# Kernel optimization log

Hardware: AMD Instinct MI355X
Metric: run time of the kernel (lower is better)

## Reference

```python
import jax, jax.numpy as jnp
import numpy as np

# tree structure: B trees, layer sizes per tree 2048 -> 256 -> 32 -> 1 (arities 8, 8, 32)
B = 256
N0, N1, N2, N3 = B * 2048, B * 256, B * 32, B * 1
D_IN, HID, OUT = 128, 256, 10
EPS = 1e-5


def _bn(x, g, b):
    # BatchNorm1d, training-mode batch stats (biased variance), as in torch
    mu = jnp.mean(x, axis=0)
    var = jnp.var(x, axis=0)
    return (x - mu) * jax.lax.rsqrt(var + EPS) * g + b


def _tree_layer(pooled, w1, b1, bn1g, bn1b, w2, b2, bng, bnb):
    # MLP(2 layers): Linear -> BN -> ReLU -> Linear, then outer BN -> ReLU (next_layer)
    z = jax.nn.relu(_bn(pooled @ w1 + b1, bn1g, bn1b))
    z = z @ w2 + b2
    return jax.nn.relu(_bn(z, bng, bnb))


def setup_inputs() -> dict:
    key = jax.random.key(0)
    ks = jax.random.split(key, 12)
    s = 0.05
    ar = lambda n: jnp.arange(n, dtype=jnp.int32)
    inp = {
        'x': jax.random.normal(ks[0], (N0, D_IN), jnp.float32),
        # child -> parent index (global, trees are contiguous blocks)
        'parent1': ar(N0) // 8,
        'parent2': ar(N1) // 8,
        'parent3': ar(N2) // 32,
        # node -> tree id per layer (for sum tree-pooling readout)
        'tree0': ar(N0) // 2048,
        'tree1': ar(N1) // 256,
        'tree2': ar(N2) // 32,
        # layer 1 MLP (input_dim -> hidden)
        'l1_w1': jax.random.normal(ks[1], (D_IN, HID), jnp.float32) * s,
        'l1_b1': jnp.zeros((HID,), jnp.float32),
        'l1_bn1g': jnp.ones((HID,), jnp.float32),
        'l1_bn1b': jnp.zeros((HID,), jnp.float32),
        'l1_w2': jax.random.normal(ks[2], (HID, HID), jnp.float32) * s,
        'l1_b2': jnp.zeros((HID,), jnp.float32),
        'l1_bng': jnp.ones((HID,), jnp.float32),
        'l1_bnb': jnp.zeros((HID,), jnp.float32),
        # layers 2 and 3 MLPs (hidden -> hidden), stacked on axis 0
        'lw1': jax.random.normal(ks[3], (2, HID, HID), jnp.float32) * s,
        'lb1': jnp.zeros((2, HID), jnp.float32),
        'lbn1g': jnp.ones((2, HID), jnp.float32),
        'lbn1b': jnp.zeros((2, HID), jnp.float32),
        'lw2': jax.random.normal(ks[4], (2, HID, HID), jnp.float32) * s,
        'lb2': jnp.zeros((2, HID), jnp.float32),
        'lbng': jnp.ones((2, HID), jnp.float32),
        'lbnb': jnp.zeros((2, HID), jnp.float32),
        # prediction heads
        'pred0_w': jax.random.normal(ks[5], (D_IN, OUT), jnp.float32) * s,
        'pred0_b': jnp.zeros((OUT,), jnp.float32),
        'predh_w': jax.random.normal(ks[6], (3, HID, OUT), jnp.float32) * s,
        'predh_b': jnp.zeros((3, OUT), jnp.float32),
    }
    return inp


def reference(x, parent1, parent2, parent3, tree0, tree1, tree2,
              l1_w1, l1_b1, l1_bn1g, l1_bn1b, l1_w2, l1_b2, l1_bng, l1_bnb,
              lw1, lb1, lbn1g, lbn1b, lw2, lb2, lbng, lbnb,
              pred0_w, pred0_b, predh_w, predh_b):
    seg = jax.ops.segment_sum
    h0 = x
    # layer 1: sparse child pooling (spmm == segment_sum) + MLP + BN + ReLU
    h1 = _tree_layer(seg(h0, parent1, num_segments=N1),
                     l1_w1, l1_b1, l1_bn1g, l1_bn1b, l1_w2, l1_b2, l1_bng, l1_bnb)
    h2 = _tree_layer(seg(h1, parent2, num_segments=N2),
                     lw1[0], lb1[0], lbn1g[0], lbn1b[0], lw2[0], lb2[0], lbng[0], lbnb[0])
    h3 = _tree_layer(seg(h2, parent3, num_segments=N3),
                     lw1[1], lb1[1], lbn1g[1], lbn1b[1], lw2[1], lb2[1], lbng[1], lbnb[1])
    # sum tree-pooling readout over layers 0..depth-1, plus root-layer linear
    score = seg(h0, tree0, num_segments=B) @ pred0_w + pred0_b
    score = score + seg(h1, tree1, num_segments=B) @ predh_w[0] + predh_b[0]
    score = score + seg(h2, tree2, num_segments=B) @ predh_w[1] + predh_b[1]
    score = score + h3 @ predh_w[2] + predh_b[2]  # h3 has 1 root per tree -> [B, OUT]
    return score
```

## Files before the change

### kernel.cpp

```cpp
#include <hip/hip_runtime.h>
#include <hip/hip_bf16.h>


#define N0 (256*2048)
#define N1 (256*256)
#define N2 (256*32)
#define NB 256
#define BN_EPS 1e-5f
#define NSLOT 8

typedef __attribute__((ext_vector_type(8))) __bf16 bf16x8;
typedef __attribute__((ext_vector_type(8))) unsigned short u16x8;
typedef __attribute__((ext_vector_type(4))) unsigned short u16x4;
typedef __attribute__((ext_vector_type(4))) float f32x4;

__device__ inline float bf2f(unsigned short b) {
    unsigned u = ((unsigned)b) << 16;
    float f; __builtin_memcpy(&f, &u, 4); return f;
}
__device__ inline unsigned short f2bf(float f) {
    unsigned u; __builtin_memcpy(&u, &f, 4);
    u += 0x7fff + ((u >> 16) & 1);
    return (unsigned short)(u >> 16);
}

__global__ __launch_bounds__(256) void prep_weights(const float* __restrict__ l1_w1,
                                                    const float* __restrict__ l1_w2,
                                                    const float* __restrict__ lw1,
                                                    const float* __restrict__ lw2,
                                                    unsigned short* __restrict__ Wt) {
    int idx = blockIdx.x * 256 + threadIdx.x;
    if (idx >= 360448) return;
    float v;
    if (idx < 32768) {
        int n = idx >> 7, k = idx & 127;
        v = l1_w1[k * 256 + n];
    } else if (idx < 98304) {
        int j = idx - 32768, n = j >> 8, k = j & 255;
        v = l1_w2[k * 256 + n];
    } else if (idx < 163840) {
        int j = idx - 98304, n = j >> 8, k = j & 255;
        v = lw1[k * 256 + n];
    } else if (idx < 229376) {
        int j = idx - 163840, n = j >> 8, k = j & 255;
        v = lw2[k * 256 + n];
    } else if (idx < 294912) {
        int j = idx - 229376, n = j >> 8, k = j & 255;
        v = lw1[65536 + k * 256 + n];
    } else {
        int j = idx - 294912, n = j >> 8, k = j & 255;
        v = lw2[65536 + k * 256 + n];
    }
    Wt[idx] = f2bf(v);
}

__device__ inline void bn_prologue(int tid, const float* __restrict__ partials,
                                   const float* __restrict__ g, const float* __restrict__ b,
                                   float invM, float* sc_lds, float* sh_lds) {
    if (tid < 256) {
        float s = 0.f, s2 = 0.f;
#pragma unroll
        for (int k = 0; k < NSLOT; ++k) {
            s  += partials[k * 512 + tid];
            s2 += partials[k * 512 + 256 + tid];
        }
        float mean = s * invM;
        float var = s2 * invM - mean * mean;
        float sc = g[tid] * rsqrtf(var + BN_EPS);
        sc_lds[tid] = sc;
        sh_lds[tid] = b[tid] - mean * sc;
    }
}

__global__ __launch_bounds__(512) void gemm1_fused(const float* __restrict__ x,
                                                   const unsigned short* __restrict__ Wt,
                                                   const float* __restrict__ bias,
                                                   unsigned short* __restrict__ Z1,
                                                   float* __restrict__ stat_partials,
                                                   float* __restrict__ ts0) {
    constexpr int LDA = 136, LDB = 72;
    __shared__ unsigned short Asb[128 * LDA];
    __shared__ unsigned short Bsb[256 * LDB];
    const int tid = threadIdx.x;
    const int c4 = tid & 31, rg = tid >> 5;
    const int m0 = blockIdx.x * 128;
    const int tree = blockIdx.x >> 1;
    f32x4 colp = {0.f, 0.f, 0.f, 0.f};
#pragma unroll
    for (int i = 0; i < 8; ++i) {
        int row = rg * 8 + i;
        const f32x4* xp = reinterpret_cast<const f32x4*>(x + (size_t)(m0 + row) * 1024 + c4 * 4);
        f32x4 s = {0.f, 0.f, 0.f, 0.f};
#pragma unroll
        for (int c = 0; c < 8; ++c) s += xp[c * 32];
        u16x4 o;
#pragma unroll
        for (int e = 0; e < 4; ++e) o[e] = f2bf(s[e]);
        *reinterpret_cast<u16x4*>(&Asb[row * LDA + c4 * 4]) = o;
        colp += s;
    }
#pragma unroll
    for (int e = 0; e < 4; ++e) atomicAdd(&ts0[tree * 128 + c4 * 4 + e], colp[e]);

    const int wave = tid >> 6, lane = tid & 63;
    const int q = lane >> 4, r = lane & 15;
    const int wc = wave & 3, wr = wave >> 2;
    f32x4 acc[4][4];
#pragma unroll
    for (int i = 0; i < 4; ++i)
#pragma unroll
        for (int j = 0; j < 4; ++j) acc[i][j] = (f32x4){0.f, 0.f, 0.f, 0.f};

#pragma unroll
    for (int s2 = 0; s2 < 2; ++s2) {
#pragma unroll
        for (int i = 0; i < 4; ++i) {
            int v = tid + i * 512;
            int n = v >> 3, kc = v & 7;
            u16x8 d = *reinterpret_cast<const u16x8*>(Wt + (size_t)n * 128 + s2 * 64 + kc * 8);
            *reinterpret_cast<u16x8*>(&Bsb[n * LDB + kc * 8]) = d;
        }
        __syncthreads();
#pragma unroll
        for (int s = 0; s < 2; ++s) {
            bf16x8 a[4], b[4];
#pragma unroll
            for (int i = 0; i < 4; ++i)
                a[i] = *reinterpret_cast<const bf16x8*>(&Asb[(wr * 64 + i * 16 + r) * LDA + s2 * 64 + s * 32 + q * 8]);
#pragma unroll
            for (int j = 0; j < 4; ++j)
                b[j] = *reinterpret_cast<const bf16x8*>(&Bsb[(wc * 64 + j * 16 + r) * LDB + s * 32 + q * 8]);
#pragma unroll
            for (int i = 0; i < 4; ++i)
#pragma unroll
                for (int j = 0; j < 4; ++j)
                    acc[i][j] = __builtin_amdgcn_mfma_f32_16x16x32_bf16(a[i], b[j], acc[i][j], 0, 0, 0);
        }
        __syncthreads();
    }
    float sj[4], s2j[4];
#pragma unroll
    for (int j = 0; j < 4; ++j) {
        float bj = bias[wc * 64 + j * 16 + r];
        float s = 0.f, s2 = 0.f;
#pragma unroll
        for (int i = 0; i < 4; ++i)
#pragma unroll
            for (int e = 0; e < 4; ++e) {
                acc[i][j][e] += bj;
                float v = acc[i][j][e];
                s += v; s2 += v * v;
            }
        s  += __shfl_xor(s, 16);  s  += __shfl_xor(s, 32);
        s2 += __shfl_xor(s2, 16); s2 += __shfl_xor(s2, 32);
        sj[j] = s; s2j[j] = s2;
    }
#pragma unroll
    for (int i = 0; i < 4; ++i)
#pragma unroll
        for (int e = 0; e < 4; ++e) {
            size_t row = m0 + wr * 64 + i * 16 + q * 4 + e;
#pragma unroll
            for (int j = 0; j < 4; ++j)
                Z1[row * 256 + wc * 64 + j * 16 + r] = f2bf(acc[i][j][e]);
        }
    if (q == 0) {
        int slot = blockIdx.x & (NSLOT - 1);
#pragma unroll
        for (int j = 0; j < 4; ++j) {
            int col = wc * 64 + j * 16 + r;
            atomicAdd(&stat_partials[slot * 512 + col], sj[j]);
            atomicAdd(&stat_partials[slot * 512 + 256 + col], s2j[j]);
        }
    }
}

__global__ __launch_bounds__(256) void gemm2_fused(const unsigned short* __restrict__ Z2,
                                                   const float* __restrict__ partials_in,
                                                   const float* __restrict__ bn_g,
                                                   const float* __restrict__ bn_b,
                                                   float invM,
                                                   const unsigned short* __restrict__ Wt2,
                                                   const float* __restrict__ bias,
                                                   unsigned short* __restrict__ Z2a,
                                                   float* __restrict__ stat_partials,
                                                   float* __restrict__ ts1) {
    constexpr int LDA = 264, LDB = 72;
    __shared__ unsigned short Asb[64 * LDA];
    __shared__ unsigned short Bsb[256 * LDB];
    __shared__ float sc_lds[256], sh_lds[256];
    const int tid = threadIdx.x;
    bn_prologue(tid, partials_in, bn_g, bn_b, invM, sc_lds, sh_lds);
    __syncthreads();
    const int c8 = tid & 31, rg = tid >> 5;
    const int m0 = blockIdx.x * 64;
    const int d0 = c8 * 8;
    float sc[8], sh[8], colp[8];
#pragma unroll
    for (int e = 0; e < 8; ++e) { sc[e] = sc_lds[d0 + e]; sh[e] = sh_lds[d0 + e]; colp[e] = 0.f; }
#pragma unroll
    for (int i = 0; i < 8; ++i) {
        int row = rg * 8 + i;
        float s[8];
#pragma unroll
        for (int e = 0; e < 8; ++e) s[e] = 0.f;
#pragma unroll
        for (int c = 0; c < 8; ++c) {
            u16x8 z = *reinterpret_cast<const u16x8*>(Z2 + ((size_t)(m0 + row) * 8 + c) * 256 + d0);
#pragma unroll
            for (int e = 0; e < 8; ++e) {
                float f = sc[e] * bf2f(z[e]) + sh[e];
                s[e] += f > 0.f ? f : 0.f;
            }
        }
        u16x8 o;
#pragma unroll
        for (int e = 0; e < 8; ++e) { o[e] = f2bf(s[e]); colp[e] += s[e]; }
        *reinterpret_cast<u16x8*>(&Asb[row * LDA + d0]) = o;
    }
    {
        int tree = blockIdx.x * 2 + (rg >> 2);
#pragma unroll
        for (int e = 0; e < 8; ++e) atomicAdd(&ts1[tree * 256 + d0 + e], colp[e]);
    }
    const int wave = tid >> 6, lane = tid & 63;
    const int q = lane >> 4, r = lane & 15;
    const int wc = wave;
    f32x4 acc[4][4];
#pragma unroll
    for (int i = 0; i < 4; ++i)
#pragma unroll
        for (int j = 0; j < 4; ++j) acc[i][j] = (f32x4){0.f, 0.f, 0.f, 0.f};

    for (int kt = 0; kt < 4; ++kt) {
#pragma unroll
        for (int i = 0; i < 8; ++i) {
            int v = tid + i * 256;
            int n = v >> 3, kc = v & 7;
            u16x8 d = *reinterpret_cast<const u16x8*>(Wt2 + (size_t)n * 256 + kt * 64 + kc * 8);
            *reinterpret_cast<u16x8*>(&Bsb[n * LDB + kc * 8]) = d;
        }
        __syncthreads();
#pragma unroll
        for (int s = 0; s < 2; ++s) {
            bf16x8 a[4], b[4];
#pragma unroll
            for (int i = 0; i < 4; ++i)
                a[i] = *reinterpret_cast<const bf16x8*>(&Asb[(i * 16 + r) * LDA + kt * 64 + s * 32 + q * 8]);
#pragma unroll
            for (int j = 0; j < 4; ++j)
                b[j] = *reinterpret_cast<const bf16x8*>(&Bsb[(wc * 64 + j * 16 + r) * LDB + s * 32 + q * 8]);
#pragma unroll
            for (int i = 0; i < 4; ++i)
#pragma unroll
                for (int j = 0; j < 4; ++j)
                    acc[i][j] = __builtin_amdgcn_mfma_f32_16x16x32_bf16(a[i], b[j], acc[i][j], 0, 0, 0);
        }
        __syncthreads();
    }
    float sj[4], s2j[4];
#pragma unroll
    for (int j = 0; j < 4; ++j) {
        float bj = bias[wc * 64 + j * 16 + r];
        float s = 0.f, s2 = 0.f;
#pragma unroll
        for (int i = 0; i < 4; ++i)
#pragma unroll
            for (int e = 0; e < 4; ++e) {
                acc[i][j][e] += bj;
                float v = acc[i][j][e];
                s += v; s2 += v * v;
            }
        s  += __shfl_xor(s, 16);  s  += __shfl_xor(s, 32);
        s2 += __shfl_xor(s2, 16); s2 += __shfl_xor(s2, 32);
        sj[j] = s; s2j[j] = s2;
    }
#pragma unroll
    for (int i = 0; i < 4; ++i)
#pragma unroll
        for (int e = 0; e < 4; ++e) {
            size_t row = m0 + i * 16 + q * 4 + e;
#pragma unroll
            for (int j = 0; j < 4; ++j)
                Z2a[row * 256 + wc * 64 + j * 16 + r] = f2bf(acc[i][j][e]);
        }
    if (q == 0) {
        int slot = blockIdx.x & (NSLOT - 1);
#pragma unroll
        for (int j = 0; j < 4; ++j) {
            int col = wc * 64 + j * 16 + r;
            atomicAdd(&stat_partials[slot * 512 + col], sj[j]);
            atomicAdd(&stat_partials[slot * 512 + 256 + col], s2j[j]);
        }
    }
}

template <int KD, bool BN_A, int BM>
__global__ __launch_bounds__(BM * 4) void mfma_gemm(const unsigned short* __restrict__ A,
                                                    const float* __restrict__ partials_in,
                                                    const float* __restrict__ bn_g,
                                                    const float* __restrict__ bn_b,
                                                    float invM,
                                                    const unsigned short* __restrict__ Wt,
                                                    const float* __restrict__ bias,
                                                    unsigned short* __restrict__ C,
                                                    float* __restrict__ stat_partials) {
    constexpr int LDA = 72;
    constexpr int NT = BM * 4;
    __shared__ unsigned short Asb[BM * LDA];
    __shared__ unsigned short Bsb[256 * LDA];
    __shared__ float sc_lds[256], sh_lds[256];
    const int tid = threadIdx.x;
    if (BN_A) {
        bn_prologue(tid, partials_in, bn_g, bn_b, invM, sc_lds, sh_lds);
        __syncthreads();
    }
    const int m0 = blockIdx.x * BM;
    const int wave = tid >> 6, lane = tid & 63;
    const int q = lane >> 4, r = lane & 15;
    const int wc = wave & 3, wr = wave >> 2;

    f32x4 acc[4][4];
#pragma unroll
    for (int i = 0; i < 4; ++i)
#pragma unroll
        for (int j = 0; j < 4; ++j) acc[i][j] = (f32x4){0.f, 0.f, 0.f, 0.f};

    for (int k0 = 0; k0 < KD; k0 += 64) {
#pragma unroll
        for (int i = 0; i < 2; ++i) {
            int v = tid + i * NT;
            int row = v >> 3, kc = v & 7;
            u16x8 d = *reinterpret_cast<const u16x8*>(A + (size_t)(m0 + row) * KD + k0 + kc * 8);
            if (BN_A) {
                u16x8 o;
#pragma unroll
                for (int e = 0; e < 8; ++e) {
                    int k = k0 + kc * 8 + e;
                    float f = sc_lds[k] * bf2f(d[e]) + sh_lds[k];
                    o[e] = f2bf(f > 0.f ? f : 0.f);
                }
                d = o;
            }
            *reinterpret_cast<u16x8*>(&Asb[row * LDA + kc * 8]) = d;
        }
#pragma unroll
        for (int i = 0; i < 2048 / NT; ++i) {
            int v = tid + i * NT;
            int n = v >> 3, kc = v & 7;
            u16x8 d = *reinterpret_cast<const u16x8*>(Wt + (size_t)n * KD + k0 + kc * 8);
            *reinterpret_cast<u16x8*>(&Bsb[n * LDA + kc * 8]) = d;
        }
        __syncthreads();
#pragma unroll
        for (int s = 0; s < 2; ++s) {
            bf16x8 a[4], b[4];
#pragma unroll
            for (int i = 0; i < 4; ++i)
                a[i] = *reinterpret_cast<const bf16x8*>(&Asb[(wr * 64 + i * 16 + r) * LDA + s * 32 + q * 8]);
#pragma unroll
            for (int j = 0; j < 4; ++j)
                b[j] = *reinterpret_cast<const bf16x8*>(&Bsb[(wc * 64 + j * 16 + r) * LDA + s * 32 + q * 8]);
#pragma unroll
            for (int i = 0; i < 4; ++i)
#pragma unroll
                for (int j = 0; j < 4; ++j)
                    acc[i][j] = __builtin_amdgcn_mfma_f32_16x16x32_bf16(a[i], b[j], acc[i][j], 0, 0, 0);
        }
        __syncthreads();
    }
    float sj[4], s2j[4];
#pragma unroll
    for (int j = 0; j < 4; ++j) {
        float bj = bias[wc * 64 + j * 16 + r];
        float s = 0.f, s2 = 0.f;
#pragma unroll
        for (int i = 0; i < 4; ++i)
#pragma unroll
            for (int e = 0; e < 4; ++e) {
                acc[i][j][e] += bj;
                float v = acc[i][j][e];
                s += v; s2 += v * v;
            }
        s  += __shfl_xor(s, 16);  s  += __shfl_xor(s, 32);
        s2 += __shfl_xor(s2, 16); s2 += __shfl_xor(s2, 32);
        sj[j] = s; s2j[j] = s2;
    }
#pragma unroll
    for (int i = 0; i < 4; ++i)
#pragma unroll
        for (int e = 0; e < 4; ++e) {
            size_t row = m0 + wr * 64 + i * 16 + q * 4 + e;
#pragma unroll
            for (int j = 0; j < 4; ++j)
                C[row * 256 + wc * 64 + j * 16 + r] = f2bf(acc[i][j][e]);
        }
    if (q == 0) {
        int slot = blockIdx.x & (NSLOT - 1);
#pragma unroll
        for (int j = 0; j < 4; ++j) {
            int col = wc * 64 + j * 16 + r;
            atomicAdd(&stat_partials[slot * 512 + col], sj[j]);
            atomicAdd(&stat_partials[slot * 512 + 256 + col], s2j[j]);
        }
    }
}

__global__ __launch_bounds__(256) void pool_bn_relu32(const unsigned short* __restrict__ Z,
                                                      const float* __restrict__ partials,
                                                      const float* __restrict__ g,
                                                      const float* __restrict__ b,
                                                      float invM,
                                                      unsigned short* __restrict__ out) {
    __shared__ float sc_lds[256], sh_lds[256];
    int tid = threadIdx.x;
    bn_prologue(tid, partials, g, b, invM, sc_lds, sh_lds);
    __syncthreads();
    int c8 = tid & 31, pl = tid >> 5;
    size_t p = (size_t)blockIdx.x * 8 + pl;
    int d0 = c8 * 8;
    float sc[8], sh[8], s[8];
#pragma unroll
    for (int e = 0; e < 8; ++e) { sc[e] = sc_lds[d0 + e]; sh[e] = sh_lds[d0 + e]; s[e] = 0.f; }
#pragma unroll
    for (int gi = 0; gi < 32; ++gi) {
        u16x8 z = *reinterpret_cast<const u16x8*>(Z + (p * 32 + gi) * 256 + d0);
#pragma unroll
        for (int e = 0; e < 8; ++e) {
            float f = sc[e] * bf2f(z[e]) + sh[e];
            s[e] += f > 0.f ? f : 0.f;
        }
    }
    u16x8 o;
#pragma unroll
    for (int e = 0; e < 8; ++e) o[e] = f2bf(s[e]);
    *reinterpret_cast<u16x8*>(out + p * 256 + d0) = o;
}

__global__ __launch_bounds__(256) void head_kernel(const float* __restrict__ ts0,
                                                   const float* __restrict__ ts1,
                                                   const unsigned short* __restrict__ p3,
                                                   const unsigned short* __restrict__ Z3b,
                                                   const float* __restrict__ partials,
                                                   const float* __restrict__ g,
                                                   const float* __restrict__ b,
                                                   float invM,
                                                   const float* __restrict__ p0w,
                                                   const float* __restrict__ p0b,
                                                   const float* __restrict__ phw,
                                                   const float* __restrict__ phb,
                                                   float* __restrict__ out) {
    __shared__ float sc_lds[256], sh_lds[256];
    int t = blockIdx.x, d = threadIdx.x;
    bn_prologue(d, partials, g, b, invM, sc_lds, sh_lds);
    __syncthreads();
    float acc[10];
#pragma unroll
    for (int o = 0; o < 10; ++o) acc[o] = 0.f;
    if (d < 128) {
        float v = ts0[t * 128 + d];
#pragma unroll
        for (int o = 0; o < 10; ++o) acc[o] += v * p0w[d * 10 + o];
    }
    {
        float v = ts1[t * 256 + d];
#pragma unroll
        for (int o = 0; o < 10; ++o) acc[o] += v * phw[d * 10 + o];
    }
    {
        float v = bf2f(p3[t * 256 + d]);
#pragma unroll
        for (int o = 0; o < 10; ++o) acc[o] += v * phw[2560 + d * 10 + o];
    }
    {
        float v = sc_lds[d] * bf2f(Z3b[t * 256 + d]) + sh_lds[d];
        v = v > 0.f ? v : 0.f;
#pragma unroll
        for (int o = 0; o < 10; ++o) acc[o] += v * phw[5120 + d * 10 + o];
    }
    __shared__ float red[256];
    for (int o = 0; o < 10; ++o) {
        red[d] = acc[o];
        __syncthreads();
        for (int s = 128; s > 0; s >>= 1) {
            if (d < s) red[d] += red[d + s];
            __syncthreads();
        }
        if (d == 0) out[t * 10 + o] = red[0] + p0b[o] + phb[o] + phb[10 + o] + phb[20 + o];
        __syncthreads();
    }
}

extern "C" void kernel_launch(void* const* d_in, const int* in_sizes, int n_in,
                              void* d_out, int out_size, void* d_ws, size_t ws_size,
                              hipStream_t stream) {
    const float* x       = (const float*)d_in[0];
    const float* l1_w1   = (const float*)d_in[7];
    const float* l1_b1   = (const float*)d_in[8];
    const float* l1_bn1g = (const float*)d_in[9];
    const float* l1_bn1b = (const float*)d_in[10];
    const float* l1_w2   = (const float*)d_in[11];
    const float* l1_b2   = (const float*)d_in[12];
    const float* l1_bng  = (const float*)d_in[13];
    const float* l1_bnb  = (const float*)d_in[14];
    const float* lw1     = (const float*)d_in[15];
    const float* lb1     = (const float*)d_in[16];
    const float* lbn1g   = (const float*)d_in[17];
    const float* lbn1b   = (const float*)d_in[18];
    const float* lw2     = (const float*)d_in[19];
    const float* lb2     = (const float*)d_in[20];
    const float* lbng    = (const float*)d_in[21];
    const float* lbnb    = (const float*)d_in[22];
    const float* pred0_w = (const float*)d_in[23];
    const float* pred0_b = (const float*)d_in[24];
    const float* predh_w = (const float*)d_in[25];
    const float* predh_b = (const float*)d_in[26];
    float* out = (float*)d_out;

    uint8_t* wsb = (uint8_t*)d_ws;
    unsigned short* Z1      = (unsigned short*)(wsb + (16ull << 20));
    unsigned short* Z2      = (unsigned short*)(wsb + (48ull << 20));
    unsigned short* Z2a     = (unsigned short*)(wsb + (84ull << 20));
    unsigned short* Z2b     = (unsigned short*)(wsb + (88ull << 20));
    unsigned short* pooled3 = (unsigned short*)(wsb + (92ull << 20));
    unsigned short* Z3a     = (unsigned short*)(wsb + (92ull << 20) + 131072);
    unsigned short* Z3b     = (unsigned short*)(wsb + (92ull << 20) + 262144);
    unsigned short* Wt      = (unsigned short*)(wsb + (93ull << 20));
    float* zbase = (float*)(wsb + (94ull << 20));
    float* ts0   = zbase;
    float* ts1   = zbase + 32768;
    float* stats = zbase + 32768 + 65536;
    auto SP = [&](int i) { return stats + i * (NSLOT * 512); };
    size_t zbytes = (32768 + 65536 + 6 * NSLOT * 512) * sizeof(float);

    hipMemsetAsync(zbase, 0, zbytes, stream);
    prep_weights<<<1408, 256, 0, stream>>>(l1_w1, l1_w2, lw1, lw2, Wt);

    gemm1_fused<<<N1 / 128, 512, 0, stream>>>(x, Wt, l1_b1, Z1, SP(0), ts0);
    mfma_gemm<256, true, 128><<<N1 / 128, 512, 0, stream>>>(
        Z1, SP(0), l1_bn1g, l1_bn1b, 1.f / N1, Wt + 32768, l1_b2, Z2, SP(1));

    gemm2_fused<<<N2 / 64, 256, 0, stream>>>(
        Z2, SP(1), l1_bng, l1_bnb, 1.f / N1, Wt + 98304, lb1, Z2a, SP(2), ts1);
    mfma_gemm<256, true, 64><<<N2 / 64, 256, 0, stream>>>(
        Z2a, SP(2), lbn1g, lbn1b, 1.f / N2, Wt + 163840, lb2, Z2b, SP(3));
    pool_bn_relu32<<<NB / 8, 256, 0, stream>>>(Z2b, SP(3), lbng, lbnb, 1.f / N2, pooled3);

    mfma_gemm<256, false, 64><<<NB / 64, 256, 0, stream>>>(
        pooled3, nullptr, nullptr, nullptr, 0.f, Wt + 229376, lb1 + 256, Z3a, SP(4));
    mfma_gemm<256, true, 64><<<NB / 64, 256, 0, stream>>>(
        Z3a, SP(4), lbn1g + 256, lbn1b + 256, 1.f / NB, Wt + 294912, lb2 + 256, Z3b, SP(5));

    head_kernel<<<NB, 256, 0, stream>>>(ts0, ts1, pooled3, Z3b, SP(5),
                                        lbng + 256, lbnb + 256, 1.f / NB,
                                        pred0_w, pred0_b, predh_w, predh_b, out);
}
```

Baseline: 191.4 us.

## Fuse post-gemm1 stages into one persistent kernel with grid barriers

Replaces the seven launches after gemm1 (the second layer-1 GEMM, layer-2 GEMMs, pooling, layer-3 GEMMs, head) with one 256-block persistent kernel. Stages are separated by atomic-counter grid barriers, and the per-tree ts1 sums are reduced in LDS instead of with atomics. This removes kernel launch gaps and tail effects on the small late stages. In exchange it relies on all 256 blocks being co-resident, since the spin barrier would deadlock otherwise, and most blocks sit idle during the tiny layer-3 stages.

```diff
diff --git a/kernel.cpp b/kernel.cpp
--- a/kernel.cpp
+++ b/kernel.cpp
@@ -54,9 +54,9 @@
     Wt[idx] = f2bf(v);
 }
 
-__device__ inline void bn_prologue(int tid, const float* __restrict__ partials,
-                                   const float* __restrict__ g, const float* __restrict__ b,
-                                   float invM, float* sc_lds, float* sh_lds) {
+__device__ __forceinline__ void bn_prologue(int tid, const float* __restrict__ partials,
+                                            const float* __restrict__ g, const float* __restrict__ b,
+                                            float invM, float* sc_lds, float* sh_lds) {
     if (tid < 256) {
         float s = 0.f, s2 = 0.f;
 #pragma unroll
@@ -70,6 +70,17 @@
         sc_lds[tid] = sc;
         sh_lds[tid] = b[tid] - mean * sc;
     }
+}
+
+__device__ __forceinline__ void gsync(int* bar, int target) {
+    __syncthreads();
+    if (threadIdx.x == 0) {
+        __threadfence();
+        __hip_atomic_fetch_add(bar, 1, __ATOMIC_ACQ_REL, __HIP_MEMORY_SCOPE_AGENT);
+        while (__hip_atomic_load(bar, __ATOMIC_RELAXED, __HIP_MEMORY_SCOPE_AGENT) < target) {}
+        __threadfence();
+    }
+    __syncthreads();
 }
 
 __global__ __launch_bounds__(512) void gemm1_fused(const float* __restrict__ x,
@@ -175,38 +186,253 @@
     }
 }
 
-__global__ __launch_bounds__(256) void gemm2_fused(const unsigned short* __restrict__ Z2,
-                                                   const float* __restrict__ partials_in,
-                                                   const float* __restrict__ bn_g,
-                                                   const float* __restrict__ bn_b,
-                                                   float invM,
-                                                   const unsigned short* __restrict__ Wt2,
-                                                   const float* __restrict__ bias,
-                                                   unsigned short* __restrict__ Z2a,
-                                                   float* __restrict__ stat_partials,
-                                                   float* __restrict__ ts1) {
-    constexpr int LDA = 264, LDB = 72;
-    __shared__ unsigned short Asb[64 * LDA];
-    __shared__ unsigned short Bsb[256 * LDB];
-    __shared__ float sc_lds[256], sh_lds[256];
+struct TailArgs {
+    const unsigned short *Z1, *Wt;
+    unsigned short *Z2, *Z2a, *Z2b, *pooled3, *Z3a, *Z3b;
+    const float *l1_bn1g, *l1_bn1b, *l1_b2, *l1_bng, *l1_bnb;
+    const float *lb1, *lbn1g, *lbn1b, *lb2, *lbng, *lbnb;
+    const float *pred0_w, *pred0_b, *predh_w, *predh_b;
+    float *ts0, *ts1, *stats, *out;
+    int *bar;
+};
+
+__device__ __forceinline__ void gemm32_kloop(const unsigned short* __restrict__ Wt,
+                                             const float* __restrict__ bias,
+                                             unsigned short* __restrict__ C,
+                                             float* __restrict__ statsOut,
+                                             int m0, int slot,
+                                             const unsigned short* Asb, unsigned short* Bsb) {
+    const int tid = threadIdx.x, wave = tid >> 6, lane = tid & 63;
+    const int q = lane >> 4, r = lane & 15;
+    const int wc = wave & 3, wr = wave >> 2;
+    f32x4 acc[4];
+#pragma unroll
+    for (int j = 0; j < 4; ++j) acc[j] = (f32x4){0.f, 0.f, 0.f, 0.f};
+    for (int kt = 0; kt < 4; ++kt) {
+#pragma unroll
+        for (int i = 0; i < 4; ++i) {
+            int v = tid + i * 512;
+            int n = v >> 3, kc = v & 7;
+            *reinterpret_cast<u16x8*>(&Bsb[n * 72 + kc * 8]) =
+                *reinterpret_cast<const u16x8*>(Wt + (size_t)n * 256 + kt * 64 + kc * 8);
+        }
+        __syncthreads();
+#pragma unroll
+        for (int s = 0; s < 2; ++s) {
+            bf16x8 a = *reinterpret_cast<const bf16x8*>(&Asb[(wr * 16 + r) * 264 + kt * 64 + s * 32 + q * 8]);
+#pragma unroll
+            for (int j = 0; j < 4; ++j) {
+                bf16x8 b = *reinterpret_cast<const bf16x8*>(&Bsb[(wc * 64 + j * 16 + r) * 72 + s * 32 + q * 8]);
+                acc[j] = __builtin_amdgcn_mfma_f32_16x16x32_bf16(a, b, acc[j], 0, 0, 0);
+            }
+        }
+        __syncthreads();
+    }
+#pragma unroll
+    for (int j = 0; j < 4; ++j) {
+        float bj = bias[wc * 64 + j * 16 + r];
+        float s = 0.f, s2 = 0.f;
+#pragma unroll
+        for (int e = 0; e < 4; ++e) {
+            acc[j][e] += bj;
+            float v = acc[j][e];
+            s += v; s2 += v * v;
+        }
+        s  += __shfl_xor(s, 16);  s  += __shfl_xor(s, 32);
+        s2 += __shfl_xor(s2, 16); s2 += __shfl_xor(s2, 32);
+#pragma unroll
+        for (int e = 0; e < 4; ++e)
+            C[(size_t)(m0 + wr * 16 + q * 4 + e) * 256 + wc * 64 + j * 16 + r] = f2bf(acc[j][e]);
+        if (q == 0) {
+            int col = wc * 64 + j * 16 + r;
+            atomicAdd(&statsOut[slot * 512 + col], s);
+            atomicAdd(&statsOut[slot * 512 + 256 + col], s2);
+        }
+    }
+}
+
+__device__ __forceinline__ void stage_A32(const unsigned short* __restrict__ A, int m0,
+                                          bool bn, const float* sc_lds, const float* sh_lds,
+                                          unsigned short* Asb) {
     const int tid = threadIdx.x;
-    bn_prologue(tid, partials_in, bn_g, bn_b, invM, sc_lds, sh_lds);
-    __syncthreads();
-    const int c8 = tid & 31, rg = tid >> 5;
-    const int m0 = blockIdx.x * 64;
-    const int d0 = c8 * 8;
-    float sc[8], sh[8], colp[8];
-#pragma unroll
-    for (int e = 0; e < 8; ++e) { sc[e] = sc_lds[d0 + e]; sh[e] = sh_lds[d0 + e]; colp[e] = 0.f; }
-#pragma unroll
-    for (int i = 0; i < 8; ++i) {
-        int row = rg * 8 + i;
-        float s[8];
-#pragma unroll
-        for (int e = 0; e < 8; ++e) s[e] = 0.f;
-#pragma unroll
-        for (int c = 0; c < 8; ++c) {
-            u16x8 z = *reinterpret_cast<const u16x8*>(Z2 + ((size_t)(m0 + row) * 8 + c) * 256 + d0);
+#pragma unroll
+    for (int i = 0; i < 2; ++i) {
+        int v = tid + i * 512;
+        int row = v >> 5, kc = v & 31;
+        u16x8 d = *reinterpret_cast<const u16x8*>(A + (size_t)(m0 + row) * 256 + kc * 8);
+        if (bn) {
+            u16x8 o;
+#pragma unroll
+            for (int e = 0; e < 8; ++e) {
+                int k = kc * 8 + e;
+                float f = sc_lds[k] * bf2f(d[e]) + sh_lds[k];
+                o[e] = f2bf(f > 0.f ? f : 0.f);
+            }
+            d = o;
+        }
+        *reinterpret_cast<u16x8*>(&Asb[row * 264 + kc * 8]) = d;
+    }
+}
+
+__global__ __launch_bounds__(512) void tail_fused(TailArgs args) {
+    __shared__ unsigned short AsbU[9216];
+    __shared__ unsigned short Bsb[256 * 72];
+    __shared__ float scsh[512];
+    const int tid = threadIdx.x, bid = blockIdx.x;
+    const int wave = tid >> 6, lane = tid & 63;
+    const int q = lane >> 4, r = lane & 15;
+    const int wc = wave & 3, wr = wave >> 2;
+    float* stats = args.stats;
+    auto SP = [&](int i) { return stats + i * (NSLOT * 512); };
+
+    bn_prologue(tid, SP(0), args.l1_bn1g, args.l1_bn1b, 1.f / N1, scsh, scsh + 256);
+    __syncthreads();
+    for (int t = 0; t < 2; ++t) {
+        const int m0 = (bid * 2 + t) * 128;
+        f32x4 acc[4][4];
+#pragma unroll
+        for (int i = 0; i < 4; ++i)
+#pragma unroll
+            for (int j = 0; j < 4; ++j) acc[i][j] = (f32x4){0.f, 0.f, 0.f, 0.f};
+        for (int kt = 0; kt < 4; ++kt) {
+#pragma unroll
+            for (int i = 0; i < 2; ++i) {
+                int v = tid + i * 512;
+                int row = v >> 3, kc = v & 7;
+                u16x8 d = *reinterpret_cast<const u16x8*>(args.Z1 + (size_t)(m0 + row) * 256 + kt * 64 + kc * 8);
+                u16x8 o;
+#pragma unroll
+                for (int e = 0; e < 8; ++e) {
+                    int k = kt * 64 + kc * 8 + e;
+                    float f = scsh[k] * bf2f(d[e]) + scsh[256 + k];
+                    o[e] = f2bf(f > 0.f ? f : 0.f);
+                }
+                *reinterpret_cast<u16x8*>(&AsbU[row * 72 + kc * 8]) = o;
+            }
+#pragma unroll
+            for (int i = 0; i < 4; ++i) {
+                int v = tid + i * 512;
+                int n = v >> 3, kc = v & 7;
+                *reinterpret_cast<u16x8*>(&Bsb[n * 72 + kc * 8]) =
+                    *reinterpret_cast<const u16x8*>(args.Wt + 32768 + (size_t)n * 256 + kt * 64 + kc * 8);
+            }
+            __syncthreads();
+#pragma unroll
+            for (int s = 0; s < 2; ++s) {
+                bf16x8 a[4], b[4];
+#pragma unroll
+                for (int i = 0; i < 4; ++i)
+                    a[i] = *reinterpret_cast<const bf16x8*>(&AsbU[(wr * 64 + i * 16 + r) * 72 + s * 32 + q * 8]);
+#pragma unroll
+                for (int j = 0; j < 4; ++j)
+                    b[j] = *reinterpret_cast<const bf16x8*>(&Bsb[(wc * 64 + j * 16 + r) * 72 + s * 32 + q * 8]);
+#pragma unroll
+                for (int i = 0; i < 4; ++i)
+#pragma unroll
+                    for (int j = 0; j < 4; ++j)
+                        acc[i][j] = __builtin_amdgcn_mfma_f32_16x16x32_bf16(a[i], b[j], acc[i][j], 0, 0, 0);
+            }
+            __syncthreads();
+        }
+        float sj[4], s2j[4];
+#pragma unroll
+        for (int j = 0; j < 4; ++j) {
+            float bj = args.l1_b2[wc * 64 + j * 16 + r];
+            float s = 0.f, s2 = 0.f;
+#pragma unroll
+            for (int i = 0; i < 4; ++i)
+#pragma unroll
+                for (int e = 0; e < 4; ++e) {
+                    acc[i][j][e] += bj;
+                    float v = acc[i][j][e];
+                    s += v; s2 += v * v;
+                }
+            s  += __shfl_xor(s, 16);  s  += __shfl_xor(s, 32);
+            s2 += __shfl_xor(s2, 16); s2 += __shfl_xor(s2, 32);
+            sj[j] = s; s2j[j] = s2;
+        }
+#pragma unroll
+        for (int i = 0; i < 4; ++i)
+#pragma unroll
+            for (int e = 0; e < 4; ++e) {
+                size_t row = m0 + wr * 64 + i * 16 + q * 4 + e;
+#pragma unroll
+                for (int j = 0; j < 4; ++j)
+                    args.Z2[row * 256 + wc * 64 + j * 16 + r] = f2bf(acc[i][j][e]);
+            }
+        if (q == 0) {
+            int slot = (bid * 2 + t) & (NSLOT - 1);
+#pragma unroll
+            for (int j = 0; j < 4; ++j) {
+                int col = wc * 64 + j * 16 + r;
+                atomicAdd(&SP(1)[slot * 512 + col], sj[j]);
+                atomicAdd(&SP(1)[slot * 512 + 256 + col], s2j[j]);
+            }
+        }
+    }
+    gsync(args.bar, 256 * 1);
+
+    bn_prologue(tid, SP(1), args.l1_bng, args.l1_bnb, 1.f / N1, scsh, scsh + 256);
+    __syncthreads();
+    {
+        const int c8 = tid & 31, rg = tid >> 5;
+        const int m0 = bid * 32, d0 = c8 * 8;
+        float sc[8], sh[8], colp[8];
+#pragma unroll
+        for (int e = 0; e < 8; ++e) { sc[e] = scsh[d0 + e]; sh[e] = scsh[256 + d0 + e]; colp[e] = 0.f; }
+#pragma unroll
+        for (int i = 0; i < 2; ++i) {
+            int row = rg * 2 + i;
+            float s[8];
+#pragma unroll
+            for (int e = 0; e < 8; ++e) s[e] = 0.f;
+#pragma unroll
+            for (int c = 0; c < 8; ++c) {
+                u16x8 z = *reinterpret_cast<const u16x8*>(args.Z2 + ((size_t)(m0 + row) * 8 + c) * 256 + d0);
+#pragma unroll
+                for (int e = 0; e < 8; ++e) {
+                    float f = sc[e] * bf2f(z[e]) + sh[e];
+                    s[e] += f > 0.f ? f : 0.f;
+                }
+            }
+            u16x8 o;
+#pragma unroll
+            for (int e = 0; e < 8; ++e) { o[e] = f2bf(s[e]); colp[e] += s[e]; }
+            *reinterpret_cast<u16x8*>(&AsbU[row * 264 + d0]) = o;
+        }
+        float* red = (float*)Bsb;
+#pragma unroll
+        for (int e = 0; e < 8; ++e) red[rg * 256 + d0 + e] = colp[e];
+        __syncthreads();
+        if (tid < 256) {
+            float t = 0.f;
+#pragma unroll
+            for (int g = 0; g < 16; ++g) t += red[g * 256 + tid];
+            args.ts1[bid * 256 + tid] = t;
+        }
+        __syncthreads();
+        gemm32_kloop(args.Wt + 98304, args.lb1, args.Z2a, SP(2), m0, bid & (NSLOT - 1), AsbU, Bsb);
+    }
+    gsync(args.bar, 256 * 2);
+
+    bn_prologue(tid, SP(2), args.lbn1g, args.lbn1b, 1.f / N2, scsh, scsh + 256);
+    __syncthreads();
+    stage_A32(args.Z2a, bid * 32, true, scsh, scsh + 256, AsbU);
+    gemm32_kloop(args.Wt + 163840, args.lb2, args.Z2b, SP(3), bid * 32, bid & (NSLOT - 1), AsbU, Bsb);
+    gsync(args.bar, 256 * 3);
+
+    bn_prologue(tid, SP(3), args.lbng, args.lbnb, 1.f / N2, scsh, scsh + 256);
+    __syncthreads();
+    if (bid < 32 && tid < 256) {
+        const int c8 = tid & 31, pl = tid >> 5;
+        size_t p = (size_t)bid * 8 + pl;
+        const int d0 = c8 * 8;
+        float sc[8], sh[8], s[8];
+#pragma unroll
+        for (int e = 0; e < 8; ++e) { sc[e] = scsh[d0 + e]; sh[e] = scsh[256 + d0 + e]; s[e] = 0.f; }
+#pragma unroll
+        for (int gi = 0; gi < 32; ++gi) {
+            u16x8 z = *reinterpret_cast<const u16x8*>(args.Z2b + (p * 32 + gi) * 256 + d0);
 #pragma unroll
             for (int e = 0; e < 8; ++e) {
                 float f = sc[e] * bf2f(z[e]) + sh[e];
@@ -215,279 +441,68 @@
         }
         u16x8 o;
 #pragma unroll
-        for (int e = 0; e < 8; ++e) { o[e] = f2bf(s[e]); colp[e] += s[e]; }
-        *reinterpret_cast<u16x8*>(&Asb[row * LDA + d0]) = o;
-    }
+        for (int e = 0; e < 8; ++e) o[e] = f2bf(s[e]);
+        *reinterpret_cast<u16x8*>(args.pooled3 + p * 256 + d0) = o;
+    }
+    gsync(args.bar, 256 * 4);
+
+    if (bid < 8) {
+        stage_A32(args.pooled3, bid * 32, false, nullptr, nullptr, AsbU);
+        gemm32_kloop(args.Wt + 229376, args.lb1 + 256, args.Z3a, SP(4), bid * 32, bid & (NSLOT - 1), AsbU, Bsb);
+    }
+    gsync(args.bar, 256 * 5);
+
+    bn_prologue(tid, SP(4), args.lbn1g + 256, args.lbn1b + 256, 1.f / NB, scsh, scsh + 256);
+    __syncthreads();
+    if (bid < 8) {
+        stage_A32(args.Z3a, bid * 32, true, scsh, scsh + 256, AsbU);
+        gemm32_kloop(args.Wt + 294912, args.lb2 + 256, args.Z3b, SP(5), bid * 32, bid & (NSLOT - 1), AsbU, Bsb);
+    }
+    gsync(args.bar, 256 * 6);
+
+    bn_prologue(tid, SP(5), args.lbng + 256, args.lbnb + 256, 1.f / NB, scsh, scsh + 256);
+    __syncthreads();
     {
-        int tree = blockIdx.x * 2 + (rg >> 2);
-#pragma unroll
-        for (int e = 0; e < 8; ++e) atomicAdd(&ts1[tree * 256 + d0 + e], colp[e]);
-    }
-    const int wave = tid >> 6, lane = tid & 63;
-    const int q = lane >> 4, r = lane & 15;
-    const int wc = wave;
-    f32x4 acc[4][4];
-#pragma unroll
-    for (int i = 0; i < 4; ++i)
-#pragma unroll
-        for (int j = 0; j < 4; ++j) acc[i][j] = (f32x4){0.f, 0.f, 0.f, 0.f};
-
-    for (int kt = 0; kt < 4; ++kt) {
-#pragma unroll
-        for (int i = 0; i < 8; ++i) {
-            int v = tid + i * 256;
-            int n = v >> 3, kc = v & 7;
-            u16x8 d = *reinterpret_cast<const u16x8*>(Wt2 + (size_t)n * 256 + kt * 64 + kc * 8);
-            *reinterpret_cast<u16x8*>(&Bsb[n * LDB + kc * 8]) = d;
-        }
-        __syncthreads();
-#pragma unroll
-        for (int s = 0; s < 2; ++s) {
-            bf16x8 a[4], b[4];
-#pragma unroll
-            for (int i = 0; i < 4; ++i)
-                a[i] = *reinterpret_cast<const bf16x8*>(&Asb[(i * 16 + r) * LDA + kt * 64 + s * 32 + q * 8]);
-#pragma unroll
-            for (int j = 0; j < 4; ++j)
-                b[j] = *reinterpret_cast<const bf16x8*>(&Bsb[(wc * 64 + j * 16 + r) * LDB + s * 32 + q * 8]);
-#pragma unroll
-            for (int i = 0; i < 4; ++i)
-#pragma unroll
-                for (int j = 0; j < 4; ++j)
-                    acc[i][j] = __builtin_amdgcn_mfma_f32_16x16x32_bf16(a[i], b[j], acc[i][j], 0, 0, 0);
-        }
-        __syncthreads();
-    }
-    float sj[4], s2j[4];
-#pragma unroll
-    for (int j = 0; j < 4; ++j) {
-        float bj = bias[wc * 64 + j * 16 + r];
-        float s = 0.f, s2 = 0.f;
-#pragma unroll
-        for (int i = 0; i < 4; ++i)
-#pragma unroll
-            for (int e = 0; e < 4; ++e) {
-                acc[i][j][e] += bj;
-                float v = acc[i][j][e];
-                s += v; s2 += v * v;
-            }
-        s  += __shfl_xor(s, 16);  s  += __shfl_xor(s, 32);
-        s2 += __shfl_xor(s2, 16); s2 += __shfl_xor(s2, 32);
-        sj[j] = s; s2j[j] = s2;
-    }
-#pragma unroll
-    for (int i = 0; i < 4; ++i)
-#pragma unroll
-        for (int e = 0; e < 4; ++e) {
-            size_t row = m0 + i * 16 + q * 4 + e;
-#pragma unroll
-            for (int j = 0; j < 4; ++j)
-                Z2a[row * 256 + wc * 64 + j * 16 + r] = f2bf(acc[i][j][e]);
-        }
-    if (q == 0) {
-        int slot = blockIdx.x & (NSLOT - 1);
-#pragma unroll
-        for (int j = 0; j < 4; ++j) {
-            int col = wc * 64 + j * 16 + r;
-            atomicAdd(&stat_partials[slot * 512 + col], sj[j]);
-            atomicAdd(&stat_partials[slot * 512 + 256 + col], s2j[j]);
-        }
-    }
-}
-
-template <int KD, bool BN_A, int BM>
-__global__ __launch_bounds__(BM * 4) void mfma_gemm(const unsigned short* __restrict__ A,
-                                                    const float* __restrict__ partials_in,
-                                                    const float* __restrict__ bn_g,
-                                                    const float* __restrict__ bn_b,
-                                                    float invM,
-                                                    const unsigned short* __restrict__ Wt,
-                                                    const float* __restrict__ bias,
-                                                    unsigned short* __restrict__ C,
-                                                    float* __restrict__ stat_partials) {
-    constexpr int LDA = 72;
-    constexpr int NT = BM * 4;
-    __shared__ unsigned short Asb[BM * LDA];
-    __shared__ unsigned short Bsb[256 * LDA];
-    __shared__ float sc_lds[256], sh_lds[256];
-    const int tid = threadIdx.x;
-    if (BN_A) {
-        bn_prologue(tid, partials_in, bn_g, bn_b, invM, sc_lds, sh_lds);
-        __syncthreads();
-    }
-    const int m0 = blockIdx.x * BM;
-    const int wave = tid >> 6, lane = tid & 63;
-    const int q = lane >> 4, r = lane & 15;
-    const int wc = wave & 3, wr = wave >> 2;
-
-    f32x4 acc[4][4];
-#pragma unroll
-    for (int i = 0; i < 4; ++i)
-#pragma unroll
-        for (int j = 0; j < 4; ++j) acc[i][j] = (f32x4){0.f, 0.f, 0.f, 0.f};
-
-    for (int k0 = 0; k0 < KD; k0 += 64) {
-#pragma unroll
-        for (int i = 0; i < 2; ++i) {
-            int v = tid + i * NT;
-            int row = v >> 3, kc = v & 7;
-            u16x8 d = *reinterpret_cast<const u16x8*>(A + (size_t)(m0 + row) * KD + k0 + kc * 8);
-            if (BN_A) {
-                u16x8 o;
-#pragma unroll
-                for (int e = 0; e < 8; ++e) {
-                    int k = k0 + kc * 8 + e;
-                    float f = sc_lds[k] * bf2f(d[e]) + sh_lds[k];
-                    o[e] = f2bf(f > 0.f ? f : 0.f);
-                }
-                d = o;
-            }
-            *reinterpret_cast<u16x8*>(&Asb[row * LDA + kc * 8]) = d;
-        }
-#pragma unroll
-        for (int i = 0; i < 2048 / NT; ++i) {
-            int v = tid + i * NT;
-            int n = v >> 3, kc = v & 7;
-            u16x8 d = *reinterpret_cast<const u16x8*>(Wt + (size_t)n * KD + k0 + kc * 8);
-            *reinterpret_cast<u16x8*>(&Bsb[n * LDA + kc * 8]) = d;
-        }
-        __syncthreads();
-#pragma unroll
-        for (int s = 0; s < 2; ++s) {
-            bf16x8 a[4], b[4];
-#pragma unroll
-            for (int i = 0; i < 4; ++i)
-                a[i] = *reinterpret_cast<const bf16x8*>(&Asb[(wr * 64 + i * 16 + r) * LDA + s * 32 + q * 8]);
-#pragma unroll
-            for (int j = 0; j < 4; ++j)
-                b[j] = *reinterpret_cast<const bf16x8*>(&Bsb[(wc * 64 + j * 16 + r) * LDA + s * 32 + q * 8]);
-#pragma unroll
-            for (int i = 0; i < 4; ++i)
-#pragma unroll
-                for (int j = 0; j < 4; ++j)
-                    acc[i][j] = __builtin_amdgcn_mfma_f32_16x16x32_bf16(a[i], b[j], acc[i][j], 0, 0, 0);
-        }
-        __syncthreads();
-    }
-    float sj[4], s2j[4];
-#pragma unroll
-    for (int j = 0; j < 4; ++j) {
-        float bj = bias[wc * 64 + j * 16 + r];
-        float s = 0.f, s2 = 0.f;
-#pragma unroll
-        for (int i = 0; i < 4; ++i)
-#pragma unroll
-            for (int e = 0; e < 4; ++e) {
-                acc[i][j][e] += bj;
-                float v = acc[i][j][e];
-                s += v; s2 += v * v;
-            }
-        s  += __shfl_xor(s, 16);  s  += __shfl_xor(s, 32);
-        s2 += __shfl_xor(s2, 16); s2 += __shfl_xor(s2, 32);
-        sj[j] = s; s2j[j] = s2;
-    }
-#pragma unroll
-    for (int i = 0; i < 4; ++i)
-#pragma unroll
-        for (int e = 0; e < 4; ++e) {
-            size_t row = m0 + wr * 64 + i * 16 + q * 4 + e;
-#pragma unroll
-            for (int j = 0; j < 4; ++j)
-                C[row * 256 + wc * 64 + j * 16 + r] = f2bf(acc[i][j][e]);
-        }
-    if (q == 0) {
-        int slot = blockIdx.x & (NSLOT - 1);
-#pragma unroll
-        for (int j = 0; j < 4; ++j) {
-            int col = wc * 64 + j * 16 + r;
-            atomicAdd(&stat_partials[slot * 512 + col], sj[j]);
-            atomicAdd(&stat_partials[slot * 512 + 256 + col], s2j[j]);
-        }
-    }
-}
-
-__global__ __launch_bounds__(256) void pool_bn_relu32(const unsigned short* __restrict__ Z,
-                                                      const float* __restrict__ partials,
-                                                      const float* __restrict__ g,
-                                                      const float* __restrict__ b,
-                                                      float invM,
-                                                      unsigned short* __restrict__ out) {
-    __shared__ float sc_lds[256], sh_lds[256];
-    int tid = threadIdx.x;
-    bn_prologue(tid, partials, g, b, invM, sc_lds, sh_lds);
-    __syncthreads();
-    int c8 = tid & 31, pl = tid >> 5;
-    size_t p = (size_t)blockIdx.x * 8 + pl;
-    int d0 = c8 * 8;
-    float sc[8], sh[8], s[8];
-#pragma unroll
-    for (int e = 0; e < 8; ++e) { sc[e] = sc_lds[d0 + e]; sh[e] = sh_lds[d0 + e]; s[e] = 0.f; }
-#pragma unroll
-    for (int gi = 0; gi < 32; ++gi) {
-        u16x8 z = *reinterpret_cast<const u16x8*>(Z + (p * 32 + gi) * 256 + d0);
-#pragma unroll
-        for (int e = 0; e < 8; ++e) {
-            float f = sc[e] * bf2f(z[e]) + sh[e];
-            s[e] += f > 0.f ? f : 0.f;
-        }
-    }
-    u16x8 o;
-#pragma unroll
-    for (int e = 0; e < 8; ++e) o[e] = f2bf(s[e]);
-    *reinterpret_cast<u16x8*>(out + p * 256 + d0) = o;
-}
-
-__global__ __launch_bounds__(256) void head_kernel(const float* __restrict__ ts0,
-                                                   const float* __restrict__ ts1,
-                                                   const unsigned short* __restrict__ p3,
-                                                   const unsigned short* __restrict__ Z3b,
-                                                   const float* __restrict__ partials,
-                                                   const float* __restrict__ g,
-                                                   const float* __restrict__ b,
-                                                   float invM,
-                                                   const float* __restrict__ p0w,
-                                                   const float* __restrict__ p0b,
-                                                   const float* __restrict__ phw,
-                                                   const float* __restrict__ phb,
-                                                   float* __restrict__ out) {
-    __shared__ float sc_lds[256], sh_lds[256];
-    int t = blockIdx.x, d = threadIdx.x;
-    bn_prologue(d, partials, g, b, invM, sc_lds, sh_lds);
-    __syncthreads();
-    float acc[10];
-#pragma unroll
-    for (int o = 0; o < 10; ++o) acc[o] = 0.f;
-    if (d < 128) {
-        float v = ts0[t * 128 + d];
-#pragma unroll
-        for (int o = 0; o < 10; ++o) acc[o] += v * p0w[d * 10 + o];
-    }
-    {
-        float v = ts1[t * 256 + d];
-#pragma unroll
-        for (int o = 0; o < 10; ++o) acc[o] += v * phw[d * 10 + o];
-    }
-    {
-        float v = bf2f(p3[t * 256 + d]);
-#pragma unroll
-        for (int o = 0; o < 10; ++o) acc[o] += v * phw[2560 + d * 10 + o];
-    }
-    {
-        float v = sc_lds[d] * bf2f(Z3b[t * 256 + d]) + sh_lds[d];
-        v = v > 0.f ? v : 0.f;
-#pragma unroll
-        for (int o = 0; o < 10; ++o) acc[o] += v * phw[5120 + d * 10 + o];
-    }
-    __shared__ float red[256];
-    for (int o = 0; o < 10; ++o) {
-        red[d] = acc[o];
-        __syncthreads();
-        for (int s = 128; s > 0; s >>= 1) {
-            if (d < s) red[d] += red[d + s];
+        const int t = bid, d = tid;
+        float acc[10];
+#pragma unroll
+        for (int o = 0; o < 10; ++o) acc[o] = 0.f;
+        if (d < 128) {
+            float v = args.ts0[t * 128 + d];
+#pragma unroll
+            for (int o = 0; o < 10; ++o) acc[o] += v * args.pred0_w[d * 10 + o];
+        }
+        if (d < 256) {
+            {
+                float v = args.ts1[t * 256 + d];
+#pragma unroll
+                for (int o = 0; o < 10; ++o) acc[o] += v * args.predh_w[d * 10 + o];
+            }
+            {
+                float v = bf2f(args.pooled3[t * 256 + d]);
+#pragma unroll
+                for (int o = 0; o < 10; ++o) acc[o] += v * args.predh_w[2560 + d * 10 + o];
+            }
+            {
+                float v = scsh[d] * bf2f(args.Z3b[t * 256 + d]) + scsh[256 + d];
+                v = v > 0.f ? v : 0.f;
+#pragma unroll
+                for (int o = 0; o < 10; ++o) acc[o] += v * args.predh_w[5120 + d * 10 + o];
+            }
+        }
+        float* red = (float*)AsbU;
+        for (int o = 0; o < 10; ++o) {
+            red[d] = (d < 256) ? acc[o] : 0.f;
             __syncthreads();
-        }
-        if (d == 0) out[t * 10 + o] = red[0] + p0b[o] + phb[o] + phb[10 + o] + phb[20 + o];
-        __syncthreads();
+            for (int s = 256; s > 0; s >>= 1) {
+                if (d < s) red[d] += red[d + s];
+                __syncthreads();
+            }
+            if (d == 0)
+                args.out[t * 10 + o] = red[0] + args.pred0_b[o] + args.predh_b[o]
+                                       + args.predh_b[10 + o] + args.predh_b[20 + o];
+            __syncthreads();
+        }
     }
 }
 
@@ -515,7 +530,6 @@
     const float* pred0_b = (const float*)d_in[24];
     const float* predh_w = (const float*)d_in[25];
     const float* predh_b = (const float*)d_in[26];
-    float* out = (float*)d_out;
 
     uint8_t* wsb = (uint8_t*)d_ws;
     unsigned short* Z1      = (unsigned short*)(wsb + (16ull << 20));
@@ -530,28 +544,23 @@
     float* ts0   = zbase;
     float* ts1   = zbase + 32768;
     float* stats = zbase + 32768 + 65536;
-    auto SP = [&](int i) { return stats + i * (NSLOT * 512); };
-    size_t zbytes = (32768 + 65536 + 6 * NSLOT * 512) * sizeof(float);
+    int*   bar   = (int*)(stats + 6 * NSLOT * 512);
+    size_t zbytes = (32768 + 65536 + 6 * NSLOT * 512) * sizeof(float) + 64;
 
     hipMemsetAsync(zbase, 0, zbytes, stream);
     prep_weights<<<1408, 256, 0, stream>>>(l1_w1, l1_w2, lw1, lw2, Wt);
-
-    gemm1_fused<<<N1 / 128, 512, 0, stream>>>(x, Wt, l1_b1, Z1, SP(0), ts0);
-    mfma_gemm<256, true, 128><<<N1 / 128, 512, 0, stream>>>(
-        Z1, SP(0), l1_bn1g, l1_bn1b, 1.f / N1, Wt + 32768, l1_b2, Z2, SP(1));
-
-    gemm2_fused<<<N2 / 64, 256, 0, stream>>>(
-        Z2, SP(1), l1_bng, l1_bnb, 1.f / N1, Wt + 98304, lb1, Z2a, SP(2), ts1);
-    mfma_gemm<256, true, 64><<<N2 / 64, 256, 0, stream>>>(
-        Z2a, SP(2), lbn1g, lbn1b, 1.f / N2, Wt + 163840, lb2, Z2b, SP(3));
-    pool_bn_relu32<<<NB / 8, 256, 0, stream>>>(Z2b, SP(3), lbng, lbnb, 1.f / N2, pooled3);
-
-    mfma_gemm<256, false, 64><<<NB / 64, 256, 0, stream>>>(
-        pooled3, nullptr, nullptr, nullptr, 0.f, Wt + 229376, lb1 + 256, Z3a, SP(4));
-    mfma_gemm<256, true, 64><<<NB / 64, 256, 0, stream>>>(
-        Z3a, SP(4), lbn1g + 256, lbn1b + 256, 1.f / NB, Wt + 294912, lb2 + 256, Z3b, SP(5));
-
-    head_kernel<<<NB, 256, 0, stream>>>(ts0, ts1, pooled3, Z3b, SP(5),
-                                        lbng + 256, lbnb + 256, 1.f / NB,
-                                        pred0_w, pred0_b, predh_w, predh_b, out);
-}
+    gemm1_fused<<<N1 / 128, 512, 0, stream>>>(x, Wt, l1_b1, Z1, stats, ts0);
+
+    TailArgs ta;
+    ta.Z1 = Z1; ta.Wt = Wt;
+    ta.Z2 = Z2; ta.Z2a = Z2a; ta.Z2b = Z2b;
+    ta.pooled3 = pooled3; ta.Z3a = Z3a; ta.Z3b = Z3b;
+    ta.l1_bn1g = l1_bn1g; ta.l1_bn1b = l1_bn1b; ta.l1_b2 = l1_b2;
+    ta.l1_bng = l1_bng; ta.l1_bnb = l1_bnb;
+    ta.lb1 = lb1; ta.lbn1g = lbn1g; ta.lbn1b = lbn1b;
+    ta.lb2 = lb2; ta.lbng = lbng; ta.lbnb = lbnb;
+    ta.pred0_w = pred0_w; ta.pred0_b = pred0_b; ta.predh_w = predh_w; ta.predh_b = predh_b;
+    ta.ts0 = ts0; ta.ts1 = ts1; ta.stats = stats; ta.out = (float*)d_out;
+    ta.bar = bar;
+    tail_fused<<<256, 512, 0, stream>>>(ta);
+}
```

Result: slower. 296.2 us (+54.7%).
